# Optimization experiments

Measured on AMD Instinct MI355X. Metric: run time of the kernel, lower is better.

Reference implementation:

```python
import jax, jax.numpy as jnp
import numpy as np

N_NODES = 50000
N_EDGES = 800000
IN_DIM = 256
HID = 256
NUM_LAYERS = 2


def _sage(xin, src, dst, inv_deg, W_l, b_l, W_r):
    # PyG SAGEConv (mean aggr): lin_l(mean of src features scattered to dst) + lin_r(x)
    agg = jax.ops.segment_sum(xin[src], dst, num_segments=xin.shape[0]) * inv_deg
    return agg @ W_l + b_l + xin @ W_r


def _mgdsgu(x, src, dst, inv_deg, h, Wx_l, bx_l, Wx_r, Wh_l, bh_l, Wh_r, Wb1, bb1, Wb2, bb2):
    # hid->hid conv order: 0=sage_hidden, 1=sage_single_h, 2=sage_update_h, 3=sage_candidate_h
    # in ->hid conv order: 0=sage_single_x, 1=sage_update_x, 2=sage_candidate_x
    h_N = _sage(h, src, dst, inv_deg, Wh_l[0], bh_l[0], Wh_r[0])
    # predict_missing_info: r = zeros so r_v = beta; gamma is computed in the
    # original but multiplied by zero -> no effect (omitted).
    beta = jnp.tanh(h @ Wb1 + bb1 + h_N @ Wb2 + bb2)
    m = h + beta - h_N
    h_N = h_N + m  # == h + beta, kept as written for clarity
    r = jax.nn.sigmoid(_sage(x, src, dst, inv_deg, Wx_l[0], bx_l[0], Wx_r[0])
                       + _sage(h_N, src, dst, inv_deg, Wh_l[1], bh_l[1], Wh_r[1]))
    z = jax.nn.sigmoid(_sage(x, src, dst, inv_deg, Wx_l[1], bx_l[1], Wx_r[1])
                       + _sage(h_N, src, dst, inv_deg, Wh_l[2], bh_l[2], Wh_r[2]))
    h_tilde = jnp.tanh(_sage(x, src, dst, inv_deg, Wx_l[2], bx_l[2], Wx_r[2])
                       + _sage(r * h_N, src, dst, inv_deg, Wh_l[3], bh_l[3], Wh_r[3]))
    return (1.0 - z) * h_N + z * h_tilde


def setup_inputs() -> dict:
    key = jax.random.key(0)
    ks = jax.random.split(key, 12)
    sx = 1.0 / np.sqrt(IN_DIM)
    sh = 1.0 / np.sqrt(HID)
    inp = {
        "x": jax.random.normal(ks[0], (N_NODES, IN_DIM), dtype=jnp.float32),
        "edge_index": jax.random.randint(ks[1], (2, N_EDGES), 0, N_NODES, dtype=jnp.int64),
        "Wx_l": jax.random.normal(ks[2], (3, IN_DIM, HID), dtype=jnp.float32) * sx,
        "bx_l": jnp.zeros((3, HID), dtype=jnp.float32),
        "Wx_r": jax.random.normal(ks[3], (3, IN_DIM, HID), dtype=jnp.float32) * sx,
        "Wh_l": jax.random.normal(ks[4], (4, HID, HID), dtype=jnp.float32) * sh,
        "bh_l": jnp.zeros((4, HID), dtype=jnp.float32),
        "Wh_r": jax.random.normal(ks[5], (4, HID, HID), dtype=jnp.float32) * sh,
        "Wb1": jax.random.normal(ks[6], (HID, HID), dtype=jnp.float32) * sh,
        "bb1": jnp.zeros((HID,), dtype=jnp.float32),
        "Wb2": jax.random.normal(ks[7], (HID, HID), dtype=jnp.float32) * sh,
        "bb2": jnp.zeros((HID,), dtype=jnp.float32),
        "We1": jax.random.normal(ks[8], (2 * HID, HID), dtype=jnp.float32) * (1.0 / np.sqrt(2 * HID)),
        "be1": jnp.zeros((HID,), dtype=jnp.float32),
        "We2": jax.random.normal(ks[9], (HID, 1), dtype=jnp.float32) * sh,
        "be2": jnp.zeros((1,), dtype=jnp.float32),
    }
    return inp


def reference(x, edge_index, Wx_l, bx_l, Wx_r, Wh_l, bh_l, Wh_r,
              Wb1, bb1, Wb2, bb2, We1, be1, We2, be2):
    src, dst = edge_index[0], edge_index[1]
    deg = jax.ops.segment_sum(jnp.ones((src.shape[0],), dtype=x.dtype), dst,
                              num_segments=x.shape[0])
    inv_deg = (1.0 / jnp.maximum(deg, 1.0))[:, None]  # [N, 1]

    h = jnp.zeros((x.shape[0], HID), dtype=x.dtype)
    for _ in range(NUM_LAYERS):
        h = _mgdsgu(x, src, dst, inv_deg, h, Wx_l, bx_l, Wx_r,
                    Wh_l, bh_l, Wh_r, Wb1, bb1, Wb2, bb2)

    # edge embeddings: concat(src emb, dst emb) -> MLP -> sigmoid
    edge_emb = jnp.concatenate([h[src], h[dst]], axis=1)  # [E, 2H]
    hidden = jax.nn.relu(edge_emb @ We1 + be1)
    preds = jax.nn.sigmoid(hidden @ We2 + be2)  # [E, 1]
    return (preds, h)
```

## Files before the change

### kernel.cpp

```cpp
#include <hip/hip_runtime.h>
#include <math.h>

#define HID 256
#define LROW 40

typedef __bf16 bf16x8 __attribute__((ext_vector_type(8)));
typedef float  f32x4  __attribute__((ext_vector_type(4)));
typedef unsigned short us8 __attribute__((ext_vector_type(8)));

__device__ __forceinline__ float sigmoidf_(float x){ return 1.0f/(1.0f + __expf(-x)); }
__device__ __forceinline__ unsigned short f2b(float f){
  __bf16 b = (__bf16)f; return __builtin_bit_cast(unsigned short, b);
}
__device__ __forceinline__ float b2f(unsigned short u){
  return (float)__builtin_bit_cast(__bf16, u);
}

__device__ __forceinline__ int edge_src(const int* ei, int e, int is64){
  return is64 ? ei[2*e] : ei[e];
}
__device__ __forceinline__ int edge_dst(const int* ei, int e, int E, int is64){
  return is64 ? ei[2*(E+e)] : ei[E+e];
}

__global__ void detect_kernel(const int* __restrict__ ei, int* __restrict__ flag){
  __shared__ int any;
  if (threadIdx.x == 0) any = 0;
  __syncthreads();
  if (ei[2*threadIdx.x + 1] != 0) atomicOr(&any, 1);
  __syncthreads();
  if (threadIdx.x == 0) *flag = any ? 0 : 1;
}

__global__ void count_kernel(const int* __restrict__ ei, const int* __restrict__ flag,
                             int* __restrict__ deg_i, int E){
  int e = blockIdx.x*blockDim.x + threadIdx.x;
  if (e >= E) return;
  int is64 = *flag;
  atomicAdd(&deg_i[edge_dst(ei,e,E,is64)], 1);
}

__global__ __launch_bounds__(1024) void scan_kernel(const int* __restrict__ deg_i,
  int* __restrict__ row_ptr, float* __restrict__ inv_deg, int N)
{
  __shared__ int wsum[16];
  __shared__ int carry_s;
  int tid = threadIdx.x, lane = tid & 63, wid = tid >> 6;
  if (tid == 0) carry_s = 0;
  __syncthreads();
  for (int base = 0; base < N; base += 1024){
    int i = base + tid;
    int v = (i < N) ? deg_i[i] : 0;
    int s = v;
    #pragma unroll
    for (int off = 1; off < 64; off <<= 1){
      int t = __shfl_up(s, off, 64);
      if (lane >= off) s += t;
    }
    if (lane == 63) wsum[wid] = s;
    __syncthreads();
    if (tid == 0){
      int run = 0;
      for (int w2 = 0; w2 < 16; ++w2){ int t = wsum[w2]; wsum[w2] = run; run += t; }
    }
    __syncthreads();
    int excl = carry_s + wsum[wid] + s - v;
    if (i < N){
      row_ptr[i] = excl;
      inv_deg[i] = 1.0f / fmaxf((float)v, 1.0f);
    }
    __syncthreads();
    if (tid == 1023) carry_s = excl + v;
    __syncthreads();
  }
  if (threadIdx.x == 0) row_ptr[N] = carry_s;
}

__global__ void fill_kernel(const int* __restrict__ ei, const int* __restrict__ flag,
                            const int* __restrict__ row_ptr, int* __restrict__ cursor,
                            int* __restrict__ col_src, int E){
  int e = blockIdx.x*blockDim.x + threadIdx.x;
  if (e >= E) return;
  int is64 = *flag;
  int d = edge_dst(ei,e,E,is64);
  int pos = atomicAdd(&cursor[d], 1);
  col_src[row_ptr[d] + pos] = edge_src(ei,e,is64);
}

__global__ __launch_bounds__(256) void conv_kernel(const float* __restrict__ in,
                                                   unsigned short* __restrict__ out, int n4){
  int i = blockIdx.x*256 + threadIdx.x;
  if (i >= n4) return;
  float4 v = *(const float4*)&in[(size_t)i*4];
  ushort4 o; o.x=f2b(v.x); o.y=f2b(v.y); o.z=f2b(v.z); o.w=f2b(v.w);
  *(ushort4*)&out[(size_t)i*4] = o;
}

__global__ __launch_bounds__(256) void wconv_kernel(
  const float* __restrict__ Wx_l, const float* __restrict__ Wx_r,
  const float* __restrict__ Wh_l, const float* __restrict__ Wh_r,
  const float* __restrict__ Wb1,  const float* __restrict__ Wb2,
  const float* __restrict__ We1,  unsigned short* __restrict__ Wt)
{
  int widx = blockIdx.x;
  int n = blockIdx.y;
  int k = threadIdx.x;
  const float* src;
  if      (widx < 3)  src = Wx_l + widx*65536;
  else if (widx < 6)  src = Wx_r + (widx-3)*65536;
  else if (widx < 10) src = Wh_l + (widx-6)*65536;
  else if (widx < 14) src = Wh_r + (widx-10)*65536;
  else if (widx == 14) src = Wb1;
  else if (widx == 15) src = Wb2;
  else                src = We1 + (widx-16)*65536;
  Wt[(size_t)widx*65536 + n*256 + k] = f2b(src[k*256 + n]);
}

__global__ __launch_bounds__(256) void comp_kernel(
  const float* __restrict__ A, const float* __restrict__ B,
  const float* __restrict__ add, unsigned short* __restrict__ dst)
{
  __shared__ float col[256];
  int n = blockIdx.x, k = threadIdx.x;
  col[k] = B[k*256 + n];
  __syncthreads();
  float s = add ? add[k*256 + n] : 0.f;
  #pragma unroll 8
  for (int j = 0; j < 256; ++j) s = fmaf(A[k*256 + j], col[j], s);
  dst[n*256 + k] = f2b(s);
}

__global__ __launch_bounds__(256) void aggregate_b_kernel(
    const unsigned short* __restrict__ X, unsigned short* __restrict__ out,
    const int* __restrict__ row_ptr, const int* __restrict__ col_src,
    const float* __restrict__ inv_deg, int N)
{
  int v = blockIdx.x*4 + (threadIdx.x >> 6);
  int lane = threadIdx.x & 63;
  if (v >= N) return;
  int beg = row_ptr[v], end = row_ptr[v+1];
  float a0=0.f, a1=0.f, a2=0.f, a3=0.f;
  int e = beg;
  for (; e + 8 <= end; e += 8){
    int sidx[8];
    #pragma unroll
    for (int t = 0; t < 8; ++t) sidx[t] = col_src[e + t];
    #pragma unroll
    for (int t = 0; t < 8; ++t){
      ushort4 u = *(const ushort4*)&X[(size_t)sidx[t]*HID + lane*4];
      a0 += b2f(u.x); a1 += b2f(u.y); a2 += b2f(u.z); a3 += b2f(u.w);
    }
  }
  for (; e < end; ++e){
    int s0 = col_src[e];
    ushort4 u = *(const ushort4*)&X[(size_t)s0*HID + lane*4];
    a0 += b2f(u.x); a1 += b2f(u.y); a2 += b2f(u.z); a3 += b2f(u.w);
  }
  float w = inv_deg[v];
  ushort4 o; o.x=f2b(a0*w); o.y=f2b(a1*w); o.z=f2b(a2*w); o.w=f2b(a3*w);
  *(ushort4*)&out[(size_t)v*HID + lane*4] = o;
}

__global__ __launch_bounds__(256) void rowprep_kernel(
  const float* __restrict__ bh_l, const float* __restrict__ bb1, const float* __restrict__ bb2,
  const float* __restrict__ Wb2, const float* __restrict__ Wh_l, const float* __restrict__ Wh_r,
  float* __restrict__ brow, float* __restrict__ hrow,
  float* __restrict__ rowL1, float* __restrict__ rowR1,
  float* __restrict__ rowL2, float* __restrict__ rowR2)
{
  __shared__ float sh[256];
  __shared__ float sh2[256];
  int j = threadIdx.x;
  sh[j] = bh_l[j];
  __syncthreads();
  float acc = bb1[j] + bb2[j];
  for (int k = 0; k < 256; ++k) acc = fmaf(sh[k], Wb2[k*256 + j], acc);
  float hr = tanhf(acc);
  brow[j] = acc;
  hrow[j] = hr; sh2[j] = hr;
  __syncthreads();
  const float* Whl1 = Wh_l + 65536;  const float* Whr1 = Wh_r + 65536;
  const float* Whl2 = Wh_l + 131072; const float* Whr2 = Wh_r + 131072;
  float a1=0.f, b1=0.f, a2=0.f, b2v=0.f;
  for (int k = 0; k < 256; ++k){
    float hv = sh2[k];
    a1  = fmaf(hv, Whl1[k*256+j], a1);
    b1  = fmaf(hv, Whr1[k*256+j], b1);
    a2  = fmaf(hv, Whl2[k*256+j], a2);
    b2v = fmaf(hv, Whr2[k*256+j], b2v);
  }
  rowL1[j] = a1; rowR1[j] = b1 + bh_l[256 + j];
  rowL2[j] = a2; rowR2[j] = b2v + bh_l[512 + j];
}

template<int MODE>
__global__ __launch_bounds__(256) void mgemm_kernel(
    const unsigned short* __restrict__ A0, const unsigned short* __restrict__ W0,
    const unsigned short* __restrict__ A1, const unsigned short* __restrict__ W1,
    const unsigned short* __restrict__ A2, const unsigned short* __restrict__ W2,
    const unsigned short* __restrict__ A3, const unsigned short* __restrict__ W3,
    const float* __restrict__ bias, const float* __restrict__ bias2,
    const float* Z, const float* HN, int hn_bcast,
    const float* __restrict__ rowA, const float* __restrict__ rowB,
    const float* __restrict__ mulrow, const float* mulmat,
    const int* __restrict__ deg,
    float* outF, unsigned short* outB, int M)
{
  __shared__ unsigned short Al[128*LROW];
  __shared__ unsigned short Bl[128*LROW];
  const int tid  = threadIdx.x;
  const int lane = tid & 63, w = tid >> 6;
  const int wr = w >> 1, wc = w & 1;
  const int lane15 = lane & 15, laneq = (lane >> 4) * 8;
  const int row0 = blockIdx.x * 128, col0 = blockIdx.y * 128;

  f32x4 acc[4][4];
  #pragma unroll
  for (int m = 0; m < 4; ++m)
    #pragma unroll
    for (int n = 0; n < 4; ++n) acc[m][n] = (f32x4)0.f;

  const unsigned short* pa[4]; const unsigned short* pw[4];
  int np = 0;
  if (A0){ pa[np]=A0; pw[np]=W0; ++np; }
  if (A1){ pa[np]=A1; pw[np]=W1; ++np; }
  if (A2){ pa[np]=A2; pw[np]=W2; ++np; }
  if (A3){ pa[np]=A3; pw[np]=W3; ++np; }
  const int steps = np * 8;

  const int srow = tid >> 1;
  const int koff = (tid & 1) * 16;
  const int arow = (row0 + srow > M-1) ? (M-1) : (row0 + srow);
  const int sidx = srow*LROW + koff;

  uint4 ra0, ra1, rb0, rb1;
  {
    const unsigned short* ga = pa[0] + (size_t)arow*HID + koff;
    const unsigned short* gb = pw[0] + (size_t)(col0 + srow)*HID + koff;
    ra0 = *(const uint4*)(ga);  ra1 = *(const uint4*)(ga + 8);
    rb0 = *(const uint4*)(gb);  rb1 = *(const uint4*)(gb + 8);
  }

  for (int s = 0; s < steps; ++s){
    __syncthreads();
    *(uint4*)&Al[sidx]     = ra0;
    *(uint4*)&Al[sidx + 8] = ra1;
    *(uint4*)&Bl[sidx]     = rb0;
    *(uint4*)&Bl[sidx + 8] = rb1;
    if (s + 1 < steps){
      int sp = s + 1;
      const unsigned short* Ap = pa[sp >> 3];
      const unsigned short* Wp = pw[sp >> 3];
      int k0 = (sp & 7) * 32;
      const unsigned short* ga = Ap + (size_t)arow*HID + k0 + koff;
      const unsigned short* gb = Wp + (size_t)(col0 + srow)*HID + k0 + koff;
      ra0 = *(const uint4*)(ga);  ra1 = *(const uint4*)(ga + 8);
      rb0 = *(const uint4*)(gb);  rb1 = *(const uint4*)(gb + 8);
    }
    __syncthreads();

    bf16x8 af[4], bfr[4];
    #pragma unroll
    for (int m = 0; m < 4; ++m)
      af[m] = *(const bf16x8*)&Al[(wr*64 + m*16 + lane15)*LROW + laneq];
    #pragma unroll
    for (int n = 0; n < 4; ++n)
      bfr[n] = *(const bf16x8*)&Bl[(wc*64 + n*16 + lane15)*LROW + laneq];
    #pragma unroll
    for (int m = 0; m < 4; ++m)
      #pragma unroll
      for (int n = 0; n < 4; ++n)
        acc[m][n] = __builtin_amdgcn_mfma_f32_16x16x32_bf16(af[m], bfr[n], acc[m][n], 0, 0, 0);
  }

  #pragma unroll
  for (int n = 0; n < 4; ++n){
    int gc = col0 + wc*64 + n*16 + lane15;
    float badd = 0.f;
    if (bias)  badd += bias[gc];
    if (bias2) badd += bias2[gc];
    float rA = 0.f, rB = 0.f, mr = 1.f, hnb = 0.f;
    if (MODE == 1){
      if (rowA){ rA = rowA[gc]; rB = rowB[gc]; }
      if (mulrow) mr = mulrow[gc];
    }
    if (MODE == 3 && hn_bcast) hnb = HN[gc];
    #pragma unroll
    for (int m = 0; m < 4; ++m){
      int rbse = row0 + wr*64 + m*16 + ((lane >> 4) << 2);
      #pragma unroll
      for (int r = 0; r < 4; ++r){
        int gr = rbse + r;
        if (gr >= M) continue;
        size_t idx = (size_t)gr*HID + gc;
        float p = acc[m][n][r] + badd;
        float v;
        if (MODE == 0) v = p;
        else if (MODE == 1){
          float g = (rowA && deg) ? ((deg[gr] > 0) ? 1.f : 0.f) : 0.f;
          v = sigmoidf_(p + g*rA + rB);
          if (mulrow) v *= mr;
          if (mulmat) v *= mulmat[idx];
        } else if (MODE == 2){
          v = HN[idx] + tanhf(p);
        } else {
          float z  = Z[idx];
          float hv = hn_bcast ? hnb : HN[idx];
          v = (1.f - z)*hv + z*tanhf(p);
        }
        if (outF) outF[idx] = v;
        if (outB) outB[idx] = f2b(v);
      }
    }
  }
}

__global__ __launch_bounds__(256) void edge_pred_kernel(
  const unsigned short* __restrict__ P, const unsigned short* __restrict__ Q,
  const int* __restrict__ ei, const int* __restrict__ flag,
  const float* __restrict__ We2, const float* __restrict__ be2,
  float* __restrict__ preds, int E)
{
  int wid = blockIdx.x*8 + (threadIdx.x >> 5);
  int l = threadIdx.x & 31;
  if (wid >= E) return;
  int is64 = *flag;
  int s = edge_src(ei, wid, is64);
  int d = edge_dst(ei, wid, E, is64);
  us8 p8 = *(const us8*)&P[(size_t)s*HID + l*8];
  us8 q8 = *(const us8*)&Q[(size_t)d*HID + l*8];
  float4 w0 = *(const float4*)&We2[l*8];
  float4 w1 = *(const float4*)&We2[l*8 + 4];
  float part = 0.f;
  #pragma unroll
  for (int j = 0; j < 4; ++j)
    part = fmaf(fmaxf(b2f(p8[j]) + b2f(q8[j]), 0.f), (&w0.x)[j], part);
  #pragma unroll
  for (int j = 0; j < 4; ++j)
    part = fmaf(fmaxf(b2f(p8[4+j]) + b2f(q8[4+j]), 0.f), (&w1.x)[j], part);
  #pragma unroll
  for (int off = 16; off > 0; off >>= 1) part += __shfl_down(part, off, 32);
  if (l == 0) preds[wid] = sigmoidf_(part + be2[0]);
}

typedef const unsigned short* cus;
typedef const float* cf;

static void launch_mg(int mode,
  cus A0, cus W0, cus A1, cus W1, cus A2, cus W2, cus A3, cus W3,
  cf bias, cf bias2, cf Z, cf HN, int hn_bcast,
  cf rowA, cf rowB, cf mulrow, cf mulmat, const int* deg,
  float* outF, unsigned short* outB, int M, hipStream_t s)
{
  dim3 g((M + 127)/128, 2), b(256);
  switch (mode){
    case 0: mgemm_kernel<0><<<g,b,0,s>>>(A0,W0,A1,W1,A2,W2,A3,W3,bias,bias2,Z,HN,hn_bcast,rowA,rowB,mulrow,mulmat,deg,outF,outB,M); break;
    case 1: mgemm_kernel<1><<<g,b,0,s>>>(A0,W0,A1,W1,A2,W2,A3,W3,bias,bias2,Z,HN,hn_bcast,rowA,rowB,mulrow,mulmat,deg,outF,outB,M); break;
    case 2: mgemm_kernel<2><<<g,b,0,s>>>(A0,W0,A1,W1,A2,W2,A3,W3,bias,bias2,Z,HN,hn_bcast,rowA,rowB,mulrow,mulmat,deg,outF,outB,M); break;
    default:mgemm_kernel<3><<<g,b,0,s>>>(A0,W0,A1,W1,A2,W2,A3,W3,bias,bias2,Z,HN,hn_bcast,rowA,rowB,mulrow,mulmat,deg,outF,outB,M); break;
  }
}

extern "C" void kernel_launch(void* const* d_in, const int* in_sizes, int n_in,
                              void* d_out, int out_size, void* d_ws, size_t ws_size,
                              hipStream_t stream)
{
  const float* x    = (const float*)d_in[0];
  const int*   ei   = (const int*)  d_in[1];
  const float* Wx_l = (const float*)d_in[2];
  const float* bx_l = (const float*)d_in[3];
  const float* Wx_r = (const float*)d_in[4];
  const float* Wh_l = (const float*)d_in[5];
  const float* bh_l = (const float*)d_in[6];
  const float* Wh_r = (const float*)d_in[7];
  const float* Wb1  = (const float*)d_in[8];
  const float* bb1  = (const float*)d_in[9];
  const float* Wb2  = (const float*)d_in[10];
  const float* bb2  = (const float*)d_in[11];
  const float* We1  = (const float*)d_in[12];
  const float* be1  = (const float*)d_in[13];
  const float* We2  = (const float*)d_in[14];
  const float* be2  = (const float*)d_in[15];

  const int N = in_sizes[0] / HID;
  const int E = in_sizes[1] / 2;
  cf NUL = nullptr; cus NUB = nullptr; const int* NULI = nullptr;

  size_t off = 0;
  auto alloc = [&](size_t bytes) -> void* {
    void* p = (char*)d_ws + off;
    off += (bytes + 255) & ~(size_t)255;
    return p;
  };
  int*   deg_i   = (int*)  alloc((size_t)N*4);
  int*   cursor  = (int*)  alloc((size_t)N*4);
  int*   row_ptr = (int*)  alloc(((size_t)N+1)*4);
  int*   col_src = (int*)  alloc((size_t)E*4);
  float* inv_deg = (float*)alloc((size_t)N*4);
  int*   flag    = (int*)  alloc(256);
  float* brow    = (float*)alloc(1024);
  float* hrow    = (float*)alloc(1024);
  float* rowL1   = (float*)alloc(1024);
  float* rowR1   = (float*)alloc(1024);
  float* rowL2   = (float*)alloc(1024);
  float* rowR2   = (float*)alloc(1024);
  unsigned short* Wt = (unsigned short*)alloc((size_t)18*65536*2);
  float* F0 = (float*)alloc((size_t)N*HID*4);
  float* F1 = (float*)alloc((size_t)N*HID*4);
  unsigned short* b0 = (unsigned short*)alloc((size_t)N*HID*2);
  unsigned short* b1 = (unsigned short*)alloc((size_t)N*HID*2);
  unsigned short* b2 = (unsigned short*)alloc((size_t)N*HID*2);
  unsigned short* b3 = (unsigned short*)alloc((size_t)N*HID*2);
  unsigned short* b4 = (unsigned short*)alloc((size_t)N*HID*2);

  float* preds = (float*)d_out;
  float* H     = preds + E;

  auto WT = [&](int i) -> cus { return Wt + (size_t)i*65536; };
  const float* bx0 = bx_l;  const float* bx1 = bx_l + 256; const float* bx2 = bx_l + 512;
  const float* bh1 = bh_l + 256;
  const float* bh2 = bh_l + 512; const float* bh3 = bh_l + 768;

  const int eb  = (E + 255)/256;
  const int nb4 = (N + 3)/4;
  const int n4b = (N*64 + 255)/256;

  hipMemsetAsync(deg_i, 0, (size_t)N*4, stream);
  hipMemsetAsync(cursor, 0, (size_t)N*4, stream);
  detect_kernel<<<1,256,0,stream>>>(ei, flag);
  count_kernel<<<eb,256,0,stream>>>(ei, flag, deg_i, E);
  scan_kernel<<<1,1024,0,stream>>>(deg_i, row_ptr, inv_deg, N);
  fill_kernel<<<eb,256,0,stream>>>(ei, flag, row_ptr, cursor, col_src, E);

  conv_kernel<<<n4b,256,0,stream>>>(x, b0, N*64);
  wconv_kernel<<<dim3(18,256),256,0,stream>>>(Wx_l, Wx_r, Wh_l, Wh_r, Wb1, Wb2, We1, Wt);
  comp_kernel<<<256,256,0,stream>>>(Wh_l, Wb2, nullptr, (unsigned short*)WT(14));
  comp_kernel<<<256,256,0,stream>>>(Wh_r, Wb2, Wb1,     (unsigned short*)WT(15));
  rowprep_kernel<<<1,256,0,stream>>>(bh_l, bb1, bb2, Wb2, Wh_l, Wh_r,
                                     brow, hrow, rowL1, rowR1, rowL2, rowR2);

  aggregate_b_kernel<<<nb4,256,0,stream>>>(b0, b1, row_ptr, col_src, inv_deg, N);
  launch_mg(1, b1,WT(0), b0,WT(3), NUB,NUB, NUB,NUB, bx0,NUL, NUL,NUL,0,
            rowL1,rowR1, hrow,NUL, deg_i, nullptr, b2, N, stream);
  launch_mg(1, b1,WT(1), b0,WT(4), NUB,NUB, NUB,NUB, bx1,NUL, NUL,NUL,0,
            rowL2,rowR2, NUL,NUL, deg_i, F0, nullptr, N, stream);
  aggregate_b_kernel<<<nb4,256,0,stream>>>(b2, b3, row_ptr, col_src, inv_deg, N);
  launch_mg(3, b3,WT(9), b2,WT(13), b1,WT(2), b0,WT(5), bx2,bh3, F0,hrow,1,
            NUL,NUL, NUL,NUL, NULI, F0, b4, N, stream);

  aggregate_b_kernel<<<nb4,256,0,stream>>>(b4, b2, row_ptr, col_src, inv_deg, N);
  launch_mg(2, b2,WT(14), b4,WT(15), NUB,NUB, NUB,NUB, brow,NUL, NUL,F0,0,
            NUL,NUL, NUL,NUL, NULI, F1, b3, N, stream);
  aggregate_b_kernel<<<nb4,256,0,stream>>>(b3, b2, row_ptr, col_src, inv_deg, N);
  launch_mg(1, b2,WT(7), b3,WT(11), b1,WT(0), b0,WT(3), bx0,bh1, NUL,NUL,0,
            NUL,NUL, NUL,F1, NULI, nullptr, b4, N, stream);
  launch_mg(1, b2,WT(8), b3,WT(12), b1,WT(1), b0,WT(4), bx1,bh2, NUL,NUL,0,
            NUL,NUL, NUL,NUL, NULI, F0, nullptr, N, stream);
  aggregate_b_kernel<<<nb4,256,0,stream>>>(b4, b2, row_ptr, col_src, inv_deg, N);
  launch_mg(3, b2,WT(9), b4,WT(13), b1,WT(2), b0,WT(5), bx2,bh3, F0,F1,0,
            NUL,NUL, NUL,NUL, NULI, H, b3, N, stream);

  launch_mg(0, b3,WT(16), NUB,NUB, NUB,NUB, NUB,NUB, be1,NUL, NUL,NUL,0,
            NUL,NUL, NUL,NUL, NULI, nullptr, b2, N, stream);
  launch_mg(0, b3,WT(17), NUB,NUB, NUB,NUB, NUB,NUB, NUL,NUL, NUL,NUL,0,
            NUL,NUL, NUL,NUL, NULI, nullptr, b4, N, stream);
  edge_pred_kernel<<<(E+7)/8,256,0,stream>>>(b2, b4, ei, flag, We2, be2, preds, E);
}
```

Before: 1.288 ms.

## Batch paired GEMM jobs into one launch and double-buffer global loads

Independent GEMM pairs (r/z gates, edge projections P/Q) are now described as job structs and run in a single launch with a doubled grid y dimension, so each launch fills more of the device. The main loop now keeps two register sets of prefetched tiles, loading step s+2 while step s computes, which gives more load latency hiding. The cost is higher register pressure, and selecting the job struct per block may add parameter or scalar overhead. Steps are always a multiple of 8, so the two-way unrolled loop stays correct.

New measurement: 1.307 ms. About the same (+1.4%).

```diff
diff --git a/kernel.cpp b/kernel.cpp
--- a/kernel.cpp
+++ b/kernel.cpp
@@ -193,26 +193,27 @@
   rowL2[j] = a2; rowR2[j] = b2v + bh_l[512 + j];
 }
 
+struct GJob {
+  const unsigned short *A0,*W0,*A1,*W1,*A2,*W2,*A3,*W3;
+  const float *bias,*bias2,*Z,*HN;
+  const float *rowA,*rowB,*mulrow,*mulmat;
+  const int* deg;
+  float* outF; unsigned short* outB;
+  int hn_bcast;
+};
+
 template<int MODE>
-__global__ __launch_bounds__(256) void mgemm_kernel(
-    const unsigned short* __restrict__ A0, const unsigned short* __restrict__ W0,
-    const unsigned short* __restrict__ A1, const unsigned short* __restrict__ W1,
-    const unsigned short* __restrict__ A2, const unsigned short* __restrict__ W2,
-    const unsigned short* __restrict__ A3, const unsigned short* __restrict__ W3,
-    const float* __restrict__ bias, const float* __restrict__ bias2,
-    const float* Z, const float* HN, int hn_bcast,
-    const float* __restrict__ rowA, const float* __restrict__ rowB,
-    const float* __restrict__ mulrow, const float* mulmat,
-    const int* __restrict__ deg,
-    float* outF, unsigned short* outB, int M)
+__global__ __launch_bounds__(256) void mgemm2_kernel(GJob j0, GJob j1, int M)
 {
   __shared__ unsigned short Al[128*LROW];
   __shared__ unsigned short Bl[128*LROW];
+  const GJob& J = (blockIdx.y >> 1) ? j1 : j0;
+  const int col0 = (blockIdx.y & 1) * 128;
   const int tid  = threadIdx.x;
   const int lane = tid & 63, w = tid >> 6;
   const int wr = w >> 1, wc = w & 1;
   const int lane15 = lane & 15, laneq = (lane >> 4) * 8;
-  const int row0 = blockIdx.x * 128, col0 = blockIdx.y * 128;
+  const int row0 = blockIdx.x * 128;
 
   f32x4 acc[4][4];
   #pragma unroll
@@ -222,43 +223,30 @@
 
   const unsigned short* pa[4]; const unsigned short* pw[4];
   int np = 0;
-  if (A0){ pa[np]=A0; pw[np]=W0; ++np; }
-  if (A1){ pa[np]=A1; pw[np]=W1; ++np; }
-  if (A2){ pa[np]=A2; pw[np]=W2; ++np; }
-  if (A3){ pa[np]=A3; pw[np]=W3; ++np; }
+  if (J.A0){ pa[np]=J.A0; pw[np]=J.W0; ++np; }
+  if (J.A1){ pa[np]=J.A1; pw[np]=J.W1; ++np; }
+  if (J.A2){ pa[np]=J.A2; pw[np]=J.W2; ++np; }
+  if (J.A3){ pa[np]=J.A3; pw[np]=J.W3; ++np; }
   const int steps = np * 8;
 
   const int srow = tid >> 1;
   const int koff = (tid & 1) * 16;
   const int arow = (row0 + srow > M-1) ? (M-1) : (row0 + srow);
+  const size_t abase = (size_t)arow*HID + koff;
+  const size_t bbase = (size_t)(col0 + srow)*HID + koff;
   const int sidx = srow*LROW + koff;
 
-  uint4 ra0, ra1, rb0, rb1;
-  {
-    const unsigned short* ga = pa[0] + (size_t)arow*HID + koff;
-    const unsigned short* gb = pw[0] + (size_t)(col0 + srow)*HID + koff;
-    ra0 = *(const uint4*)(ga);  ra1 = *(const uint4*)(ga + 8);
-    rb0 = *(const uint4*)(gb);  rb1 = *(const uint4*)(gb + 8);
-  }
-
-  for (int s = 0; s < steps; ++s){
-    __syncthreads();
-    *(uint4*)&Al[sidx]     = ra0;
-    *(uint4*)&Al[sidx + 8] = ra1;
-    *(uint4*)&Bl[sidx]     = rb0;
-    *(uint4*)&Bl[sidx + 8] = rb1;
-    if (s + 1 < steps){
-      int sp = s + 1;
-      const unsigned short* Ap = pa[sp >> 3];
-      const unsigned short* Wp = pw[sp >> 3];
-      int k0 = (sp & 7) * 32;
-      const unsigned short* ga = Ap + (size_t)arow*HID + k0 + koff;
-      const unsigned short* gb = Wp + (size_t)(col0 + srow)*HID + k0 + koff;
-      ra0 = *(const uint4*)(ga);  ra1 = *(const uint4*)(ga + 8);
-      rb0 = *(const uint4*)(gb);  rb1 = *(const uint4*)(gb + 8);
-    }
-    __syncthreads();
-
+  uint4 A0a,A0b,B0a,B0b, A1a,A1b,B1a,B1b;
+  auto loadR = [&](int sp, uint4& a0, uint4& a1, uint4& b0, uint4& b1){
+    const unsigned short* Ap = pa[sp >> 3];
+    const unsigned short* Wp = pw[sp >> 3];
+    const int k0 = (sp & 7) * 32;
+    const unsigned short* ga = Ap + abase + k0;
+    const unsigned short* gb = Wp + bbase + k0;
+    a0 = *(const uint4*)ga;  a1 = *(const uint4*)(ga + 8);
+    b0 = *(const uint4*)gb;  b1 = *(const uint4*)(gb + 8);
+  };
+  auto compute = [&](){
     bf16x8 af[4], bfr[4];
     #pragma unroll
     for (int m = 0; m < 4; ++m)
@@ -271,20 +259,37 @@
       #pragma unroll
       for (int n = 0; n < 4; ++n)
         acc[m][n] = __builtin_amdgcn_mfma_f32_16x16x32_bf16(af[m], bfr[n], acc[m][n], 0, 0, 0);
+  };
+
+  loadR(0, A0a,A0b,B0a,B0b);
+  loadR(1, A1a,A1b,B1a,B1b);
+  for (int s = 0; s < steps; s += 2){
+    __syncthreads();
+    *(uint4*)&Al[sidx] = A0a; *(uint4*)&Al[sidx+8] = A0b;
+    *(uint4*)&Bl[sidx] = B0a; *(uint4*)&Bl[sidx+8] = B0b;
+    __syncthreads();
+    if (s + 2 < steps) loadR(s+2, A0a,A0b,B0a,B0b);
+    compute();
+    __syncthreads();
+    *(uint4*)&Al[sidx] = A1a; *(uint4*)&Al[sidx+8] = A1b;
+    *(uint4*)&Bl[sidx] = B1a; *(uint4*)&Bl[sidx+8] = B1b;
+    __syncthreads();
+    if (s + 3 < steps) loadR(s+3, A1a,A1b,B1a,B1b);
+    compute();
   }
 
   #pragma unroll
   for (int n = 0; n < 4; ++n){
     int gc = col0 + wc*64 + n*16 + lane15;
     float badd = 0.f;
-    if (bias)  badd += bias[gc];
-    if (bias2) badd += bias2[gc];
+    if (J.bias)  badd += J.bias[gc];
+    if (J.bias2) badd += J.bias2[gc];
     float rA = 0.f, rB = 0.f, mr = 1.f, hnb = 0.f;
     if (MODE == 1){
-      if (rowA){ rA = rowA[gc]; rB = rowB[gc]; }
-      if (mulrow) mr = mulrow[gc];
-    }
-    if (MODE == 3 && hn_bcast) hnb = HN[gc];
+      if (J.rowA){ rA = J.rowA[gc]; rB = J.rowB[gc]; }
+      if (J.mulrow) mr = J.mulrow[gc];
+    }
+    if (MODE == 3 && J.hn_bcast) hnb = J.HN[gc];
     #pragma unroll
     for (int m = 0; m < 4; ++m){
       int rbse = row0 + wr*64 + m*16 + ((lane >> 4) << 2);
@@ -297,19 +302,19 @@
         float v;
         if (MODE == 0) v = p;
         else if (MODE == 1){
-          float g = (rowA && deg) ? ((deg[gr] > 0) ? 1.f : 0.f) : 0.f;
+          float g = (J.rowA && J.deg) ? ((J.deg[gr] > 0) ? 1.f : 0.f) : 0.f;
           v = sigmoidf_(p + g*rA + rB);
-          if (mulrow) v *= mr;
-          if (mulmat) v *= mulmat[idx];
+          if (J.mulrow) v *= mr;
+          if (J.mulmat) v *= J.mulmat[idx];
         } else if (MODE == 2){
-          v = HN[idx] + tanhf(p);
+          v = J.HN[idx] + tanhf(p);
         } else {
-          float z  = Z[idx];
-          float hv = hn_bcast ? hnb : HN[idx];
+          float z  = J.Z[idx];
+          float hv = J.hn_bcast ? hnb : J.HN[idx];
           v = (1.f - z)*hv + z*tanhf(p);
         }
-        if (outF) outF[idx] = v;
-        if (outB) outB[idx] = f2b(v);
+        if (J.outF) J.outF[idx] = v;
+        if (J.outB) J.outB[idx] = f2b(v);
       }
     }
   }
@@ -346,19 +351,10 @@
 typedef const unsigned short* cus;
 typedef const float* cf;
 
-static void launch_mg(int mode,
-  cus A0, cus W0, cus A1, cus W1, cus A2, cus W2, cus A3, cus W3,
-  cf bias, cf bias2, cf Z, cf HN, int hn_bcast,
-  cf rowA, cf rowB, cf mulrow, cf mulmat, const int* deg,
-  float* outF, unsigned short* outB, int M, hipStream_t s)
-{
-  dim3 g((M + 127)/128, 2), b(256);
-  switch (mode){
-    case 0: mgemm_kernel<0><<<g,b,0,s>>>(A0,W0,A1,W1,A2,W2,A3,W3,bias,bias2,Z,HN,hn_bcast,rowA,rowB,mulrow,mulmat,deg,outF,outB,M); break;
-    case 1: mgemm_kernel<1><<<g,b,0,s>>>(A0,W0,A1,W1,A2,W2,A3,W3,bias,bias2,Z,HN,hn_bcast,rowA,rowB,mulrow,mulmat,deg,outF,outB,M); break;
-    case 2: mgemm_kernel<2><<<g,b,0,s>>>(A0,W0,A1,W1,A2,W2,A3,W3,bias,bias2,Z,HN,hn_bcast,rowA,rowB,mulrow,mulmat,deg,outF,outB,M); break;
-    default:mgemm_kernel<3><<<g,b,0,s>>>(A0,W0,A1,W1,A2,W2,A3,W3,bias,bias2,Z,HN,hn_bcast,rowA,rowB,mulrow,mulmat,deg,outF,outB,M); break;
-  }
+template<int MODE>
+static void launch_fused(const GJob& a, const GJob* b, int M, hipStream_t s){
+  dim3 g((M + 127)/128, b ? 4 : 2), blk(256);
+  mgemm2_kernel<MODE><<<g, blk, 0, s>>>(a, b ? *b : a, M);
 }
 
 extern "C" void kernel_launch(void* const* d_in, const int* in_sizes, int n_in,
@@ -425,6 +421,18 @@
   const int nb4 = (N + 3)/4;
   const int n4b = (N*64 + 255)/256;
 
+  auto mkjob = [&](cus A0,cus W0,cus A1,cus W1,cus A2,cus W2,cus A3,cus W3,
+                   cf bias, cf bias2, cf Z, cf HN, int hnb,
+                   cf rA, cf rB, cf mr, cf mm, const int* dg,
+                   float* oF, unsigned short* oB) -> GJob {
+    GJob g;
+    g.A0=A0; g.W0=W0; g.A1=A1; g.W1=W1; g.A2=A2; g.W2=W2; g.A3=A3; g.W3=W3;
+    g.bias=bias; g.bias2=bias2; g.Z=Z; g.HN=HN; g.hn_bcast=hnb;
+    g.rowA=rA; g.rowB=rB; g.mulrow=mr; g.mulmat=mm; g.deg=dg;
+    g.outF=oF; g.outB=oB;
+    return g;
+  };
+
   hipMemsetAsync(deg_i, 0, (size_t)N*4, stream);
   hipMemsetAsync(cursor, 0, (size_t)N*4, stream);
   detect_kernel<<<1,256,0,stream>>>(ei, flag);
@@ -440,29 +448,47 @@
                                      brow, hrow, rowL1, rowR1, rowL2, rowR2);
 
   aggregate_b_kernel<<<nb4,256,0,stream>>>(b0, b1, row_ptr, col_src, inv_deg, N);
-  launch_mg(1, b1,WT(0), b0,WT(3), NUB,NUB, NUB,NUB, bx0,NUL, NUL,NUL,0,
-            rowL1,rowR1, hrow,NUL, deg_i, nullptr, b2, N, stream);
-  launch_mg(1, b1,WT(1), b0,WT(4), NUB,NUB, NUB,NUB, bx1,NUL, NUL,NUL,0,
-            rowL2,rowR2, NUL,NUL, deg_i, F0, nullptr, N, stream);
+  {
+    GJob jt = mkjob(b1,WT(0), b0,WT(3), NUB,NUB, NUB,NUB, bx0,NUL, NUL,NUL,0,
+                    rowL1,rowR1, hrow,NUL, deg_i, nullptr, b2);
+    GJob jz = mkjob(b1,WT(1), b0,WT(4), NUB,NUB, NUB,NUB, bx1,NUL, NUL,NUL,0,
+                    rowL2,rowR2, NUL,NUL, deg_i, F0, nullptr);
+    launch_fused<1>(jt, &jz, N, stream);
+  }
   aggregate_b_kernel<<<nb4,256,0,stream>>>(b2, b3, row_ptr, col_src, inv_deg, N);
-  launch_mg(3, b3,WT(9), b2,WT(13), b1,WT(2), b0,WT(5), bx2,bh3, F0,hrow,1,
-            NUL,NUL, NUL,NUL, NULI, F0, b4, N, stream);
+  {
+    GJob jh = mkjob(b3,WT(9), b2,WT(13), b1,WT(2), b0,WT(5), bx2,bh3, F0,hrow,1,
+                    NUL,NUL, NUL,NUL, NULI, F0, b4);
+    launch_fused<3>(jh, nullptr, N, stream);
+  }
 
   aggregate_b_kernel<<<nb4,256,0,stream>>>(b4, b2, row_ptr, col_src, inv_deg, N);
-  launch_mg(2, b2,WT(14), b4,WT(15), NUB,NUB, NUB,NUB, brow,NUL, NUL,F0,0,
-            NUL,NUL, NUL,NUL, NULI, F1, b3, N, stream);
+  {
+    GJob jn = mkjob(b2,WT(14), b4,WT(15), NUB,NUB, NUB,NUB, brow,NUL, NUL,F0,0,
+                    NUL,NUL, NUL,NUL, NULI, F1, b3);
+    launch_fused<2>(jn, nullptr, N, stream);
+  }
   aggregate_b_kernel<<<nb4,256,0,stream>>>(b3, b2, row_ptr, col_src, inv_deg, N);
-  launch_mg(1, b2,WT(7), b3,WT(11), b1,WT(0), b0,WT(3), bx0,bh1, NUL,NUL,0,
-            NUL,NUL, NUL,F1, NULI, nullptr, b4, N, stream);
-  launch_mg(1, b2,WT(8), b3,WT(12), b1,WT(1), b0,WT(4), bx1,bh2, NUL,NUL,0,
-            NUL,NUL, NUL,NUL, NULI, F0, nullptr, N, stream);
+  {
+    GJob jt = mkjob(b2,WT(7), b3,WT(11), b1,WT(0), b0,WT(3), bx0,bh1, NUL,NUL,0,
+                    NUL,NUL, NUL,F1, NULI, nullptr, b4);
+    GJob jz = mkjob(b2,WT(8), b3,WT(12), b1,WT(1), b0,WT(4), bx1,bh2, NUL,NUL,0,
+                    NUL,NUL, NUL,NUL, NULI, F0, nullptr);
+    launch_fused<1>(jt, &jz, N, stream);
+  }
   aggregate_b_kernel<<<nb4,256,0,stream>>>(b4, b2, row_ptr, col_src, inv_deg, N);
-  launch_mg(3, b2,WT(9), b4,WT(13), b1,WT(2), b0,WT(5), bx2,bh3, F0,F1,0,
-            NUL,NUL, NUL,NUL, NULI, H, b3, N, stream);
-
-  launch_mg(0, b3,WT(16), NUB,NUB, NUB,NUB, NUB,NUB, be1,NUL, NUL,NUL,0,
-            NUL,NUL, NUL,NUL, NULI, nullptr, b2, N, stream);
-  launch_mg(0, b3,WT(17), NUB,NUB, NUB,NUB, NUB,NUB, NUL,NUL, NUL,NUL,0,
-            NUL,NUL, NUL,NUL, NULI, nullptr, b4, N, stream);
+  {
+    GJob jh = mkjob(b2,WT(9), b4,WT(13), b1,WT(2), b0,WT(5), bx2,bh3, F0,F1,0,
+                    NUL,NUL, NUL,NUL, NULI, H, b3);
+    launch_fused<3>(jh, nullptr, N, stream);
+  }
+
+  {
+    GJob jp = mkjob(b3,WT(16), NUB,NUB, NUB,NUB, NUB,NUB, be1,NUL, NUL,NUL,0,
+                    NUL,NUL, NUL,NUL, NULI, nullptr, b2);
+    GJob jq = mkjob(b3,WT(17), NUB,NUB, NUB,NUB, NUB,NUB, NUL,NUL, NUL,NUL,0,
+                    NUL,NUL, NUL,NUL, NULI, nullptr, b4);
+    launch_fused<0>(jp, &jq, N, stream);
+  }
   edge_pred_kernel<<<(E+7)/8,256,0,stream>>>(b2, b4, ei, flag, We2, be2, preds, E);
 }
```
